# Performance work log

Hardware: AMD Instinct MI355X
Metric: run time of the kernel (lower is better)

Reference implementation:

```python
import jax, jax.numpy as jnp
import numpy as np

B = 32768        # batch
S = 256          # subnet_num
H1, H2 = 10, 6   # subnet_arch
L2_SMOOTH = 1e-3
EPS = 1e-10


def setup_inputs() -> dict:
    key = jax.random.key(0)
    k = jax.random.split(key, 7)
    def glorot(kk, shape, fan_in, fan_out):
        return (jax.random.normal(kk, shape, jnp.float32)
                * np.float32(np.sqrt(2.0 / (fan_in + fan_out))))
    x = jax.random.normal(k[0], (B, S), jnp.float32)
    W1 = glorot(k[1], (S, 1, H1), 1, H1)
    b1 = jnp.zeros((S, H1), jnp.float32)
    W2 = glorot(k[2], (S, H1, H2), H1, H2)
    b2 = jnp.zeros((S, H2), jnp.float32)
    W3 = glorot(k[3], (S, H2, 1), H2, 1)
    b3 = jnp.zeros((S, 1), jnp.float32)
    return {"x": x, "W1": W1, "b1": b1, "W2": W2, "b2": b2, "W3": W3, "b3": b3}


def _mlp_scalar(xs, W1, b1, W2, b2, W3, b3):
    # xs: scalar input of one subnet for one sample
    h = jnp.tanh(xs * W1[0] + b1)   # [H1]
    h = jnp.tanh(h @ W2 + b2)       # [H2]
    return (h @ W3 + b3)[0]         # scalar


def _per_subnet(fn):
    # inner vmap over batch (x axis 0, params broadcast), outer over subnets
    inner = jax.vmap(fn, in_axes=(0, None, None, None, None, None, None))
    return jax.vmap(inner, in_axes=(1, 0, 0, 0, 0, 0, 0))  # -> [S, B]


def reference(x, W1, b1, W2, b2, W3, b3):
    out = _per_subnet(_mlp_scalar)(x, W1, b1, W2, b2, W3, b3)           # [S, B]
    d2f = jax.grad(jax.grad(_mlp_scalar))                               # Hessian diag (scalar input)
    g2 = _per_subnet(d2f)(x, W1, b1, W2, b2, W3, b3)                    # [S, B]
    # training-mode batch stats (population std, as tf.math.reduce_std)
    mean = jnp.mean(out, axis=1, keepdims=True)                         # [S, 1]
    std = jnp.maximum(jnp.std(out, axis=1, keepdims=True), EPS)         # [S, 1]
    out_bn = ((out - mean) / std).T                                     # [B, S]
    smooth_loss = L2_SMOOTH * jnp.sum(jnp.mean(g2 * g2, axis=1) / std[:, 0])
    return out_bn, smooth_loss
```

## Files before the change

### kernel.cpp

```cpp
#include <hip/hip_runtime.h>
#include <math.h>

#define B 32768
#define S 256
#define H1 10
#define H2 6
#define ST 16
#define CB 1024
#define RB 256
#define PAD 20
#define NCHUNK (B / CB)
#define L2_SMOOTH 1e-3f
#define EPS 1e-10f

__device__ __forceinline__ float rfl(float x) {
    return __int_as_float(__builtin_amdgcn_readfirstlane(__float_as_int(x)));
}

__device__ __forceinline__ void tanh_pair(float x, float& th, float& s2) {
    const float e = __builtin_amdgcn_exp2f(x * 2.885390081777927f);
    const float r = __builtin_amdgcn_rcpf(e + 1.0f);
    th = fmaf(-2.0f, r, 1.0f);
    s2 = (4.0f * r) * (1.0f - r);
}

__global__ __launch_bounds__(1024, 4) void k1_mlp(
    const float* __restrict__ x,
    const float* __restrict__ W1, const float* __restrict__ b1,
    const float* __restrict__ W2, const float* __restrict__ b2,
    const float* __restrict__ W3, const float* __restrict__ b3,
    float* __restrict__ out,
    float* __restrict__ psum,
    float* __restrict__ psum2,
    float* __restrict__ pg2)
{
    __shared__ float xlds[RB * PAD];
    __shared__ float olds[RB * PAD];

    const int t  = threadIdx.x;
    const int wv = __builtin_amdgcn_readfirstlane(t >> 6);
    const int l  = t & 63;
    const int s0 = blockIdx.x * ST;
    const int s  = s0 + wv;
    const int bbase = blockIdx.y * CB;

    float w1[H1], bb1[H1], w2s[H1][H2], bb2[H2], w3[H2];
#pragma unroll
    for (int i = 0; i < H1; ++i) { w1[i] = W1[s * H1 + i]; bb1[i] = b1[s * H1 + i]; }
#pragma unroll
    for (int i = 0; i < H1; ++i)
#pragma unroll
        for (int j = 0; j < H2; ++j) w2s[i][j] = rfl(W2[(s * H1 + i) * H2 + j]);
#pragma unroll
    for (int j = 0; j < H2; ++j) { bb2[j] = rfl(b2[s * H2 + j]); w3[j] = rfl(W3[s * H2 + j]); }
    const float bb3 = rfl(b3[s]);
    float w1m2[H1];
#pragma unroll
    for (int i = 0; i < H1; ++i) w1m2[i] = -2.0f * w1[i] * w1[i];

    const int brow = t >> 2;
    const int s4   = (t & 3) * 4;

    float so = 0.0f, so2 = 0.0f, sg2 = 0.0f;

    for (int r = 0; r < CB / RB; ++r) {
        const float4 xv = *reinterpret_cast<const float4*>(
            &x[(bbase + r * RB + brow) * S + s0 + s4]);
        *reinterpret_cast<float4*>(&xlds[brow * PAD + s4]) = xv;
        __syncthreads();

#pragma unroll
        for (int k = 0; k < RB / 64; ++k) {
            const float xs = xlds[(k * 64 + l) * PAD + wv];

            float v[H2], vp[H2], vpp[H2];
#pragma unroll
            for (int j = 0; j < H2; ++j) { v[j] = bb2[j]; vp[j] = 0.0f; vpp[j] = 0.0f; }

#pragma unroll
            for (int i = 0; i < H1; ++i) {
                float h, tt;
                tanh_pair(fmaf(xs, w1[i], bb1[i]), h, tt);
                const float hp  = tt * w1[i];
                const float hpp = (h * tt) * w1m2[i];
#pragma unroll
                for (int j = 0; j < H2; ++j) {
                    v[j]   = fmaf(h,   w2s[i][j], v[j]);
                    vp[j]  = fmaf(hp,  w2s[i][j], vp[j]);
                    vpp[j] = fmaf(hpp, w2s[i][j], vpp[j]);
                }
            }

            float o = bb3, g2 = 0.0f;
#pragma unroll
            for (int j = 0; j < H2; ++j) {
                float g, tg;
                tanh_pair(v[j], g, tg);
                const float c   = -2.0f * (g * vp[j]);
                const float gpp = tg * fmaf(c, vp[j], vpp[j]);
                o  = fmaf(g,     w3[j], o);
                g2 = fmaf(w3[j], gpp,   g2);
            }

            olds[(k * 64 + l) * PAD + wv] = o;
            so += o; so2 = fmaf(o, o, so2); sg2 = fmaf(g2, g2, sg2);
        }
        __syncthreads();

        const float4 ov = *reinterpret_cast<const float4*>(&olds[brow * PAD + s4]);
        *reinterpret_cast<float4*>(&out[(bbase + r * RB + brow) * S + s0 + s4]) = ov;
    }

#pragma unroll
    for (int m = 1; m < 64; m <<= 1) {
        so  += __shfl_xor(so,  m, 64);
        so2 += __shfl_xor(so2, m, 64);
        sg2 += __shfl_xor(sg2, m, 64);
    }
    if (l == 0) {
        psum [s * NCHUNK + blockIdx.y] = so;
        psum2[s * NCHUNK + blockIdx.y] = so2;
        pg2  [s * NCHUNK + blockIdx.y] = sg2;
    }
}

__global__ __launch_bounds__(256) void k2_reduce(
    const float* __restrict__ psum, const float* __restrict__ psum2,
    const float* __restrict__ pg2,
    float* __restrict__ mean_arr, float* __restrict__ rstd_arr,
    float* __restrict__ smooth_arr)
{
    const int s = blockIdx.x;
    const int t = threadIdx.x;

    float a = 0.0f, b_ = 0.0f, c = 0.0f;
    if (t < NCHUNK) {
        a  = psum [s * NCHUNK + t];
        b_ = psum2[s * NCHUNK + t];
        c  = pg2  [s * NCHUNK + t];
    }

    __shared__ float sa[256], sb[256], sc[256];
    sa[t] = a; sb[t] = b_; sc[t] = c;
    __syncthreads();
    for (int st = 128; st > 0; st >>= 1) {
        if (t < st) { sa[t] += sa[t + st]; sb[t] += sb[t + st]; sc[t] += sc[t + st]; }
        __syncthreads();
    }

    if (t == 0) {
        const float inv_b = 1.0f / (float)B;
        const float mean  = sa[0] * inv_b;
        float var = sb[0] * inv_b - mean * mean;
        var = fmaxf(var, 0.0f);
        const float stdv = fmaxf(sqrtf(var), EPS);
        const float rstd = 1.0f / stdv;
        mean_arr[s]   = mean;
        rstd_arr[s]   = rstd;
        smooth_arr[s] = (sc[0] * inv_b) * rstd;
    }
}

#define K3_NORM_BLOCKS (B * S / (256 * 4))
__global__ __launch_bounds__(256) void k3_norm(
    float* __restrict__ out,
    const float* __restrict__ mean_arr, const float* __restrict__ rstd_arr,
    const float* __restrict__ smooth_arr)
{
    if ((int)blockIdx.x == K3_NORM_BLOCKS) {
        const int t = threadIdx.x;
        __shared__ float sa[256];
        sa[t] = smooth_arr[t];
        __syncthreads();
        for (int st = 128; st > 0; st >>= 1) {
            if (t < st) sa[t] += sa[t + st];
            __syncthreads();
        }
        if (t == 0) out[B * S] = L2_SMOOTH * sa[0];
        return;
    }

    const int i4   = (int)blockIdx.x * 256 + (int)threadIdx.x;
    const int base = i4 * 4;
    float4 v = *reinterpret_cast<float4*>(&out[base]);
    const int s0 = base & (S - 1);
    v.x = (v.x - mean_arr[s0 + 0]) * rstd_arr[s0 + 0];
    v.y = (v.y - mean_arr[s0 + 1]) * rstd_arr[s0 + 1];
    v.z = (v.z - mean_arr[s0 + 2]) * rstd_arr[s0 + 2];
    v.w = (v.w - mean_arr[s0 + 3]) * rstd_arr[s0 + 3];
    *reinterpret_cast<float4*>(&out[base]) = v;
}

extern "C" void kernel_launch(void* const* d_in, const int* in_sizes, int n_in,
                              void* d_out, int out_size, void* d_ws, size_t ws_size,
                              hipStream_t stream) {
    const float* x  = (const float*)d_in[0];
    const float* W1 = (const float*)d_in[1];
    const float* b1 = (const float*)d_in[2];
    const float* W2 = (const float*)d_in[3];
    const float* b2 = (const float*)d_in[4];
    const float* W3 = (const float*)d_in[5];
    const float* b3 = (const float*)d_in[6];
    float* out = (float*)d_out;

    float* psum   = (float*)d_ws;
    float* psum2  = psum  + S * NCHUNK;
    float* pg2    = psum2 + S * NCHUNK;
    float* meanA  = pg2   + S * NCHUNK;
    float* rstdA  = meanA + S;
    float* smooth = rstdA + S;

    k1_mlp<<<dim3(S / ST, NCHUNK), 1024, 0, stream>>>(
        x, W1, b1, W2, b2, W3, b3, out, psum, psum2, pg2);
    k2_reduce<<<S, 256, 0, stream>>>(psum, psum2, pg2, meanA, rstdA, smooth);
    k3_norm<<<K3_NORM_BLOCKS + 1, 256, 0, stream>>>(out, meanA, rstdA, smooth);
}
```

Measured before the change: 120.3 us.

## Drop LDS staging: one wave per subnet-chunk with strided direct global access

Reworks k1 so that each wave handles one subnet over a 512-row chunk and reads x and writes out directly from global memory with stride S. This removes the LDS transpose and the __syncthreads barriers. The change also peels the first loop iterations to save FMAs and shortens hpp by reusing hp. k2 now reduces its 64 partials with a wave shuffle instead of an LDS tree. The cost is uncoalesced 4-byte global accesses with a 1KB stride across lanes, which may hurt memory efficiency, though neighbouring waves touch adjacent columns and may share cache lines in L2.

```diff
diff --git a/kernel.cpp b/kernel.cpp
--- a/kernel.cpp
+++ b/kernel.cpp
@@ -5,14 +5,13 @@
 #define S 256
 #define H1 10
 #define H2 6
-#define ST 16
-#define CB 1024
-#define RB 256
-#define PAD 20
-#define NCHUNK (B / CB)
+#define ROWS 512
+#define CH (B / ROWS)
+#define WPB 4
 #define L2_SMOOTH 1e-3f
 #define EPS 1e-10f
 
+__device__ __forceinline__ int rfl_i(int x) { return __builtin_amdgcn_readfirstlane(x); }
 __device__ __forceinline__ float rfl(float x) {
     return __int_as_float(__builtin_amdgcn_readfirstlane(__float_as_int(x)));
 }
@@ -24,7 +23,7 @@
     s2 = (4.0f * r) * (1.0f - r);
 }
 
-__global__ __launch_bounds__(1024, 4) void k1_mlp(
+__global__ __launch_bounds__(256, 6) void k1_mlp(
     const float* __restrict__ x,
     const float* __restrict__ W1, const float* __restrict__ b1,
     const float* __restrict__ W2, const float* __restrict__ b2,
@@ -34,81 +33,90 @@
     float* __restrict__ psum2,
     float* __restrict__ pg2)
 {
-    __shared__ float xlds[RB * PAD];
-    __shared__ float olds[RB * PAD];
-
-    const int t  = threadIdx.x;
-    const int wv = __builtin_amdgcn_readfirstlane(t >> 6);
-    const int l  = t & 63;
-    const int s0 = blockIdx.x * ST;
-    const int s  = s0 + wv;
-    const int bbase = blockIdx.y * CB;
-
-    float w1[H1], bb1[H1], w2s[H1][H2], bb2[H2], w3[H2];
-#pragma unroll
-    for (int i = 0; i < H1; ++i) { w1[i] = W1[s * H1 + i]; bb1[i] = b1[s * H1 + i]; }
+    const int t   = threadIdx.x;
+    const int wid = blockIdx.x * WPB + rfl_i(t >> 6);
+    const int l   = t & 63;
+    const int s   = wid & (S - 1);
+    const int c   = wid >> 8;
+
+    float w1[H1], bb1[H1], m2w1[H1], w2s[H1][H2], bb2[H2], w3s[H2];
+#pragma unroll
+    for (int i = 0; i < H1; ++i) {
+        w1[i]   = W1[s * H1 + i];
+        bb1[i]  = b1[s * H1 + i];
+        m2w1[i] = -2.0f * w1[i];
+    }
 #pragma unroll
     for (int i = 0; i < H1; ++i)
 #pragma unroll
         for (int j = 0; j < H2; ++j) w2s[i][j] = rfl(W2[(s * H1 + i) * H2 + j]);
 #pragma unroll
-    for (int j = 0; j < H2; ++j) { bb2[j] = rfl(b2[s * H2 + j]); w3[j] = rfl(W3[s * H2 + j]); }
-    const float bb3 = rfl(b3[s]);
-    float w1m2[H1];
-#pragma unroll
-    for (int i = 0; i < H1; ++i) w1m2[i] = -2.0f * w1[i] * w1[i];
-
-    const int brow = t >> 2;
-    const int s4   = (t & 3) * 4;
+    for (int j = 0; j < H2; ++j) {
+        bb2[j] = b2[s * H2 + j];
+        asm("" : "+v"(bb2[j]));
+        w3s[j] = rfl(W3[s * H2 + j]);
+    }
+    float bb3 = b3[s];
+    asm("" : "+v"(bb3));
+
+    const size_t base = (size_t)(c * ROWS) * S + s;
+    const float* px = x   + base;
+    float*       po = out + base;
+    const int loff = l * S;
 
     float so = 0.0f, so2 = 0.0f, sg2 = 0.0f;
 
-    for (int r = 0; r < CB / RB; ++r) {
-        const float4 xv = *reinterpret_cast<const float4*>(
-            &x[(bbase + r * RB + brow) * S + s0 + s4]);
-        *reinterpret_cast<float4*>(&xlds[brow * PAD + s4]) = xv;
-        __syncthreads();
-
-#pragma unroll
-        for (int k = 0; k < RB / 64; ++k) {
-            const float xs = xlds[(k * 64 + l) * PAD + wv];
-
-            float v[H2], vp[H2], vpp[H2];
-#pragma unroll
-            for (int j = 0; j < H2; ++j) { v[j] = bb2[j]; vp[j] = 0.0f; vpp[j] = 0.0f; }
-
-#pragma unroll
-            for (int i = 0; i < H1; ++i) {
-                float h, tt;
-                tanh_pair(fmaf(xs, w1[i], bb1[i]), h, tt);
-                const float hp  = tt * w1[i];
-                const float hpp = (h * tt) * w1m2[i];
-#pragma unroll
-                for (int j = 0; j < H2; ++j) {
-                    v[j]   = fmaf(h,   w2s[i][j], v[j]);
-                    vp[j]  = fmaf(hp,  w2s[i][j], vp[j]);
-                    vpp[j] = fmaf(hpp, w2s[i][j], vpp[j]);
-                }
+    for (int k = 0; k < ROWS / 64; ++k) {
+        const float xs = px[k * 64 * S + loff];
+
+        float v[H2], vp[H2], vpp[H2];
+        {
+            float h, tt;
+            tanh_pair(fmaf(xs, w1[0], bb1[0]), h, tt);
+            const float hp  = tt * w1[0];
+            const float hpp = (h * hp) * m2w1[0];
+#pragma unroll
+            for (int j = 0; j < H2; ++j) {
+                v[j]   = fmaf(h, w2s[0][j], bb2[j]);
+                vp[j]  = hp  * w2s[0][j];
+                vpp[j] = hpp * w2s[0][j];
             }
-
-            float o = bb3, g2 = 0.0f;
+        }
+#pragma unroll
+        for (int i = 1; i < H1; ++i) {
+            float h, tt;
+            tanh_pair(fmaf(xs, w1[i], bb1[i]), h, tt);
+            const float hp  = tt * w1[i];
+            const float hpp = (h * hp) * m2w1[i];
 #pragma unroll
             for (int j = 0; j < H2; ++j) {
-                float g, tg;
-                tanh_pair(v[j], g, tg);
-                const float c   = -2.0f * (g * vp[j]);
-                const float gpp = tg * fmaf(c, vp[j], vpp[j]);
-                o  = fmaf(g,     w3[j], o);
-                g2 = fmaf(w3[j], gpp,   g2);
+                v[j]   = fmaf(h,   w2s[i][j], v[j]);
+                vp[j]  = fmaf(hp,  w2s[i][j], vp[j]);
+                vpp[j] = fmaf(hpp, w2s[i][j], vpp[j]);
             }
-
-            olds[(k * 64 + l) * PAD + wv] = o;
-            so += o; so2 = fmaf(o, o, so2); sg2 = fmaf(g2, g2, sg2);
-        }
-        __syncthreads();
-
-        const float4 ov = *reinterpret_cast<const float4*>(&olds[brow * PAD + s4]);
-        *reinterpret_cast<float4*>(&out[(bbase + r * RB + brow) * S + s0 + s4]) = ov;
+        }
+
+        float o, g2;
+        {
+            float g, tg;
+            tanh_pair(v[0], g, tg);
+            const float c0  = -2.0f * (g * vp[0]);
+            const float gpp = tg * fmaf(c0, vp[0], vpp[0]);
+            o  = fmaf(g, w3s[0], bb3);
+            g2 = gpp * w3s[0];
+        }
+#pragma unroll
+        for (int j = 1; j < H2; ++j) {
+            float g, tg;
+            tanh_pair(v[j], g, tg);
+            const float cj  = -2.0f * (g * vp[j]);
+            const float gpp = tg * fmaf(cj, vp[j], vpp[j]);
+            o  = fmaf(g,     w3s[j], o);
+            g2 = fmaf(w3s[j], gpp,   g2);
+        }
+
+        po[k * 64 * S + loff] = o;
+        so += o; so2 = fmaf(o, o, so2); sg2 = fmaf(g2, g2, sg2);
     }
 
 #pragma unroll
@@ -118,46 +126,40 @@
         sg2 += __shfl_xor(sg2, m, 64);
     }
     if (l == 0) {
-        psum [s * NCHUNK + blockIdx.y] = so;
-        psum2[s * NCHUNK + blockIdx.y] = so2;
-        pg2  [s * NCHUNK + blockIdx.y] = sg2;
-    }
-}
-
-__global__ __launch_bounds__(256) void k2_reduce(
+        psum [s * CH + c] = so;
+        psum2[s * CH + c] = so2;
+        pg2  [s * CH + c] = sg2;
+    }
+}
+
+__global__ __launch_bounds__(64) void k2_reduce(
     const float* __restrict__ psum, const float* __restrict__ psum2,
     const float* __restrict__ pg2,
     float* __restrict__ mean_arr, float* __restrict__ rstd_arr,
     float* __restrict__ smooth_arr)
 {
     const int s = blockIdx.x;
-    const int t = threadIdx.x;
-
-    float a = 0.0f, b_ = 0.0f, c = 0.0f;
-    if (t < NCHUNK) {
-        a  = psum [s * NCHUNK + t];
-        b_ = psum2[s * NCHUNK + t];
-        c  = pg2  [s * NCHUNK + t];
-    }
-
-    __shared__ float sa[256], sb[256], sc[256];
-    sa[t] = a; sb[t] = b_; sc[t] = c;
-    __syncthreads();
-    for (int st = 128; st > 0; st >>= 1) {
-        if (t < st) { sa[t] += sa[t + st]; sb[t] += sb[t + st]; sc[t] += sc[t + st]; }
-        __syncthreads();
-    }
-
-    if (t == 0) {
+    const int l = threadIdx.x;
+
+    float a  = psum [s * CH + l];
+    float b_ = psum2[s * CH + l];
+    float cc = pg2  [s * CH + l];
+#pragma unroll
+    for (int m = 1; m < 64; m <<= 1) {
+        a  += __shfl_xor(a,  m, 64);
+        b_ += __shfl_xor(b_, m, 64);
+        cc += __shfl_xor(cc, m, 64);
+    }
+    if (l == 0) {
         const float inv_b = 1.0f / (float)B;
-        const float mean  = sa[0] * inv_b;
-        float var = sb[0] * inv_b - mean * mean;
+        const float mean  = a * inv_b;
+        float var = b_ * inv_b - mean * mean;
         var = fmaxf(var, 0.0f);
         const float stdv = fmaxf(sqrtf(var), EPS);
         const float rstd = 1.0f / stdv;
         mean_arr[s]   = mean;
         rstd_arr[s]   = rstd;
-        smooth_arr[s] = (sc[0] * inv_b) * rstd;
+        smooth_arr[s] = (cc * inv_b) * rstd;
     }
 }
 
@@ -204,14 +206,14 @@
     float* out = (float*)d_out;
 
     float* psum   = (float*)d_ws;
-    float* psum2  = psum  + S * NCHUNK;
-    float* pg2    = psum2 + S * NCHUNK;
-    float* meanA  = pg2   + S * NCHUNK;
+    float* psum2  = psum  + S * CH;
+    float* pg2    = psum2 + S * CH;
+    float* meanA  = pg2   + S * CH;
     float* rstdA  = meanA + S;
     float* smooth = rstdA + S;
 
-    k1_mlp<<<dim3(S / ST, NCHUNK), 1024, 0, stream>>>(
+    k1_mlp<<<S * CH / WPB, 64 * WPB, 0, stream>>>(
         x, W1, b1, W2, b2, W3, b3, out, psum, psum2, pg2);
-    k2_reduce<<<S, 256, 0, stream>>>(psum, psum2, pg2, meanA, rstdA, smooth);
+    k2_reduce<<<S, 64, 0, stream>>>(psum, psum2, pg2, meanA, rstdA, smooth);
     k3_norm<<<K3_NORM_BLOCKS + 1, 256, 0, stream>>>(out, meanA, rstdA, smooth);
 }
```

New measurement: 113.6 us. -5.6%, faster.
